# Kernel tuning notes

Hardware: AMD Instinct MI355X
Metric: run time of the kernel (lower is better)

Reference implementation:

```python
import jax, jax.numpy as jnp
import numpy as np

EPS = 1e-6
D_MODEL, D_HEAD, COND_F = 1024, 64, 768
N_HEADS = D_MODEL // D_HEAD
BATCH, SEQ = 2, 2048


def _rope_freqs(d_head, n_heads):
    # RoPE.__init__: dim = d_head // 2; count = n_heads * dim // 4 = n_heads * d_head // 8
    d8 = d_head // 8
    log_min, log_max = np.log(np.pi), np.log(10.0 * np.pi)
    f = np.exp(np.linspace(log_min, log_max, n_heads * d8 + 1, dtype=np.float64)[:-1])
    return jnp.asarray(f.reshape(d8, n_heads).T, dtype=jnp.float32)  # [nh, d8]


def _apply_rotary(x, theta):
    # x: [n, nh, l, e], theta: [n, nh, l, d8]; rotate first 2*d8 channels
    d = theta.shape[-1]
    x1, x2, rest = x[..., :d], x[..., d:2 * d], x[..., 2 * d:]
    cos, sin = jnp.cos(theta), jnp.sin(theta)
    y1 = x1 * cos - x2 * sin
    y2 = x2 * cos + x1 * sin
    return jnp.concatenate([y1, y2, rest], axis=-1)


def setup_inputs() -> dict:
    key = jax.random.key(0)
    ks = jax.random.split(key, 6)
    x = jax.random.normal(ks[0], (BATCH, SEQ, D_MODEL), dtype=jnp.float32)
    pos = jnp.broadcast_to(jnp.arange(SEQ, dtype=jnp.float32), (BATCH, SEQ))[..., None]
    cond = jax.random.normal(ks[1], (BATCH, COND_F), dtype=jnp.float32)
    w_norm = jax.random.normal(ks[2], (D_MODEL, COND_F), dtype=jnp.float32) * 0.02
    w_qkv = jax.random.normal(ks[3], (3 * D_MODEL, D_MODEL), dtype=jnp.float32) * 0.02
    scale = jnp.full((N_HEADS,), 10.0, dtype=jnp.float32)
    w_out = jax.random.normal(ks[4], (D_MODEL, D_MODEL), dtype=jnp.float32) * 0.02
    return {"x": x, "pos": pos, "cond": cond, "w_norm": w_norm,
            "w_qkv": w_qkv, "scale": scale, "w_out": w_out}


def reference(x, pos, cond, w_norm, w_qkv, scale, w_out):
    n, l, d = x.shape
    nh, e = N_HEADS, D_HEAD
    skip = x
    # AdaRMSNorm: scale = (linear(cond) + 1) * rsqrt(mean(x^2))
    cond_scale = cond @ w_norm.T + 1.0                      # [n, d]
    mean_sq = jnp.mean(x * x, axis=-1, keepdims=True)       # [n, l, 1]
    xn = x * (cond_scale[:, None, :] * jax.lax.rsqrt(mean_sq + EPS))
    # QKV projection
    qkv = (xn @ w_qkv.T).reshape(n, l, 3, nh, e)
    q = jnp.transpose(qkv[:, :, 0], (0, 2, 1, 3))           # [n, nh, l, e]
    k = jnp.transpose(qkv[:, :, 1], (0, 2, 1, 3))
    v = jnp.transpose(qkv[:, :, 2], (0, 2, 1, 3))
    # cosine-sim scaling
    sqrt_scale = jnp.sqrt(scale)[None, :, None, None]       # [1, nh, 1, 1]
    q = q * (sqrt_scale * jax.lax.rsqrt(jnp.sum(q * q, axis=-1, keepdims=True) + EPS))
    k = k * (sqrt_scale * jax.lax.rsqrt(jnp.sum(k * k, axis=-1, keepdims=True) + EPS))
    # RoPE: theta = pos[..., None] * freqs -> [n, l, nh, d8] -> [n, nh, l, d8]
    freqs = _rope_freqs(e, nh)
    theta = jnp.transpose(pos[..., None] * freqs, (0, 2, 1, 3))
    q = _apply_rotary(q, theta)
    k = _apply_rotary(k, theta)
    # attention with softmax scale = 1.0
    scores = jnp.einsum('nhle,nhme->nhlm', q, k)
    attn = jax.nn.softmax(scores, axis=-1)
    out = jnp.einsum('nhlm,nhme->nhle', attn, v)
    out = jnp.transpose(out, (0, 2, 1, 3)).reshape(n, l, d)
    return out @ w_out.T + skip
```

## Files before the change

kernel.cpp:

```cpp
#include <hip/hip_runtime.h>
#include <math.h>

#define D_MODEL 1024
#define D_HEAD  64
#define N_HEADS 16
#define COND_F  768
#define BATCH   2
#define SEQ     2048
#define NTOK    (BATCH*SEQ)
#define QKV_N   (3*D_MODEL)

typedef unsigned short u16;
typedef __attribute__((ext_vector_type(4))) float  f32x4;
typedef __attribute__((ext_vector_type(8))) __bf16 bfrag;
typedef __attribute__((ext_vector_type(4))) unsigned short u16x4;
typedef __attribute__((ext_vector_type(8))) unsigned short u16x8;

__device__ __forceinline__ u16 f2bf(float f) {
    unsigned u = __builtin_bit_cast(unsigned, f);
    return (u16)((u + 0x7fffu + ((u >> 16) & 1u)) >> 16);
}
__device__ __forceinline__ float bf2f(u16 h) {
    unsigned u = ((unsigned)h) << 16;
    return __builtin_bit_cast(float, u);
}

__device__ __forceinline__ float fexp2(float x) {
    float y;
    asm("v_exp_f32 %0, %1" : "=v"(y) : "v"(x));
    return y;
}

__device__ __forceinline__ void async16(const void* g, void* l) {
    __builtin_amdgcn_global_load_lds(
        (const __attribute__((address_space(1))) unsigned int*)g,
        (__attribute__((address_space(3))) unsigned int*)l, 16, 0, 0);
}

#define SBAR do { __builtin_amdgcn_sched_barrier(0); \
                  __builtin_amdgcn_s_barrier(); \
                  __builtin_amdgcn_sched_barrier(0); } while (0)
#define WAITV4 do { asm volatile("s_waitcnt vmcnt(4)" ::: "memory"); } while (0)
#define WAITV2 do { asm volatile("s_waitcnt vmcnt(2)" ::: "memory"); } while (0)
#define WAITV0 do { asm volatile("s_waitcnt vmcnt(0)" ::: "memory"); } while (0)

__global__ __launch_bounds__(256) void prep_kernel(const float* __restrict__ wqkv,
                                                   const float* __restrict__ wout,
                                                   u16* __restrict__ wqkv_b,
                                                   u16* __restrict__ wout_b,
                                                   const float* __restrict__ cond,
                                                   const float* __restrict__ w_norm,
                                                   float* __restrict__ cs,
                                                   const float* __restrict__ pos,
                                                   float2* __restrict__ tab) {
    if (blockIdx.x < 2048) {
        int i = blockIdx.x * 256 + threadIdx.x;
        const int n1 = QKV_N * D_MODEL / 8;
        const float* src; u16* dst; int off;
        if (i < n1) { src = wqkv; dst = wqkv_b; off = i * 8; }
        else        { src = wout; dst = wout_b; off = (i - n1) * 8; }
        float4 a = *(const float4*)(src + off);
        float4 b = *(const float4*)(src + off + 4);
        *(u16x4*)(dst + off)     = (u16x4){f2bf(a.x), f2bf(a.y), f2bf(a.z), f2bf(a.w)};
        *(u16x4*)(dst + off + 4) = (u16x4){f2bf(b.x), f2bf(b.y), f2bf(b.z), f2bf(b.w)};
    } else if (blockIdx.x < 2560) {
        int lane = threadIdx.x & 63, w = threadIdx.x >> 6;
        int wid = (blockIdx.x - 2048) * 4 + w;
        int b = wid >> 10, d = wid & 1023;
        const float* c = cond + b * COND_F;
        const float* wn = w_norm + (size_t)d * COND_F;
        float acc = 0.f;
        #pragma unroll
        for (int kk = 0; kk < 3; ++kk) {
            int j = kk * 256 + lane * 4;
            float4 cv = *(const float4*)(c + j);
            float4 wv = *(const float4*)(wn + j);
            acc += cv.x * wv.x + cv.y * wv.y + cv.z * wv.z + cv.w * wv.w;
        }
        for (int m = 1; m < 64; m <<= 1) acc += __shfl_xor(acc, m);
        if (lane == 0) cs[wid] = acc + 1.0f;
    } else {
        int i = (blockIdx.x - 2560) * 256 + threadIdx.x;
        int j = i & 7, h = (i >> 3) & 15;
        int s = (i >> 7) & 2047, b = i >> 18;
        double lf = 1.1447298858494001741 + (double)(j * 16 + h) * (2.302585092994045684 / 128.0);
        float fr = (float)exp(lf);
        float th = pos[b * SEQ + s] * fr;
        tab[i] = make_float2(cosf(th), sinf(th));
    }
}

__global__ __launch_bounds__(256) void rmsnorm_kernel(const float* __restrict__ x,
                                                      const float* __restrict__ cs,
                                                      u16* __restrict__ xn) {
    int tok = blockIdx.x, t = threadIdx.x;
    int b = tok >> 11;
    const float* xr = x + (size_t)tok * D_MODEL;
    float4 v = *(const float4*)(xr + t * 4);
    float ss = v.x * v.x + v.y * v.y + v.z * v.z + v.w * v.w;
    for (int m = 1; m < 64; m <<= 1) ss += __shfl_xor(ss, m);
    __shared__ float red[4];
    int w = t >> 6;
    if ((t & 63) == 0) red[w] = ss;
    __syncthreads();
    float tot = red[0] + red[1] + red[2] + red[3];
    float r = rsqrtf(tot * (1.0f / D_MODEL) + 1e-6f);
    float4 cv = *(const float4*)(cs + b * D_MODEL + t * 4);
    *(u16x4*)(xn + (size_t)tok * D_MODEL + t * 4) =
        (u16x4){f2bf(v.x * cv.x * r), f2bf(v.y * cv.y * r),
                f2bf(v.z * cv.z * r), f2bf(v.w * cv.w * r)};
}

__global__ __launch_bounds__(256) void gemm_qkv(const u16* __restrict__ A, const u16* __restrict__ B,
                                                u16* __restrict__ Cq, u16* __restrict__ Ck,
                                                u16* __restrict__ Cv,
                                                const float* __restrict__ scale,
                                                const float2* __restrict__ tab,
                                                int M, int N, int K) {
    __shared__ u16 As0[128 * 32];
    __shared__ u16 As1[128 * 32];
    __shared__ u16 Bs0[128 * 32];
    __shared__ u16 Bs1[128 * 32];
    int tid = threadIdx.x;
    int lane = tid & 63, w = tid >> 6;
    int wr = w >> 1, wc = w & 1;
    int m0 = blockIdx.x * 128, n0 = blockIdx.y * 128;
    f32x4 acc[4][4] = {};
    const u16* Ag = A + (size_t)m0 * K;
    const u16* Bg = B + (size_t)n0 * K;
    int lr = lane & 15, lq = lane >> 4;

    #define GSTAGE(kt, Ad, Bd) do { \
        _Pragma("unroll") \
        for (int i = 0; i < 2; ++i) { \
            int c = i * 256 + tid; int row = c >> 2, col = (c & 3) * 8; \
            async16(Ag + (size_t)row * K + (kt) + col, Ad + c * 8); \
            async16(Bg + (size_t)row * K + (kt) + col, Bd + c * 8); \
        } } while (0)

    auto compute = [&](const u16* Asb, const u16* Bsb) {
        bfrag af[4], bfv[4];
        #pragma unroll
        for (int fm = 0; fm < 4; ++fm)
            af[fm] = *(const bfrag*)&Asb[(wr * 64 + fm * 16 + lr) * 32 + lq * 8];
        #pragma unroll
        for (int fn = 0; fn < 4; ++fn)
            bfv[fn] = *(const bfrag*)&Bsb[(wc * 64 + fn * 16 + lr) * 32 + lq * 8];
        #pragma unroll
        for (int fm = 0; fm < 4; ++fm)
            #pragma unroll
            for (int fn = 0; fn < 4; ++fn)
                acc[fm][fn] = __builtin_amdgcn_mfma_f32_16x16x32_bf16(af[fm], bfv[fn], acc[fm][fn], 0, 0, 0);
    };

    const int NK = K / 32;
    GSTAGE(0, As0, Bs0);
    GSTAGE(32, As1, Bs1);

    for (int t = 0; t < NK; t += 2) {
        if (t + 1 < NK) WAITV4; else WAITV0;
        SBAR;
        compute(As0, Bs0);
        SBAR;
        if (t + 2 < NK) GSTAGE((size_t)(t + 2) * 32, As0, Bs0);
        if (t + 1 < NK) {
            if (t + 2 < NK) WAITV4; else WAITV0;
            SBAR;
            compute(As1, Bs1);
            SBAR;
            if (t + 3 < NK) GSTAGE((size_t)(t + 3) * 32, As1, Bs1);
        }
    }
    #undef GSTAGE

    #pragma unroll
    for (int fn_dummy = 0; fn_dummy < 1; ++fn_dummy) {
        int colbase0 = n0 + wc * 64;
        int sel = colbase0 >> 10;
        int h = (colbase0 >> 6) & 15;
        int bb = m0 >> 11;
        if (sel == 2) {
            #pragma unroll
            for (int fm = 0; fm < 4; ++fm) {
                int sP = (m0 & 2047) + wr * 64 + (fm >> 1) * 32 + 8 * lq + 4 * (fm & 1);
                #pragma unroll
                for (int fn = 0; fn < 4; ++fn) {
                    int e = fn * 16 + lr;
                    u16x4 pk = {f2bf(acc[fm][fn][0]), f2bf(acc[fm][fn][1]),
                                f2bf(acc[fm][fn][2]), f2bf(acc[fm][fn][3])};
                    *(u16x4*)&Cv[((size_t)(bb * N_HEADS + h) * D_HEAD + e) * SEQ + sP] = pk;
                }
            }
        } else {
            u16* p = sel ? Ck : Cq;
            float sq = sqrtf(scale[h]);
            float mult = (sel == 0) ? sq * 1.4426950408889634f : sq;
            #pragma unroll
            for (int fm = 0; fm < 4; ++fm) {
                int s0 = (m0 & 2047) + wr * 64 + fm * 16 + lq * 4;
                #pragma unroll
                for (int r = 0; r < 4; ++r) {
                    float v0 = acc[fm][0][r], v1 = acc[fm][1][r],
                          v2 = acc[fm][2][r], v3 = acc[fm][3][r];
                    float ss = v0 * v0 + v1 * v1 + v2 * v2 + v3 * v3;
                    ss += __shfl_xor(ss, 1); ss += __shfl_xor(ss, 2);
                    ss += __shfl_xor(ss, 4); ss += __shfl_xor(ss, 8);
                    float rs = mult * rsqrtf(ss + 1e-6f);
                    v0 *= rs; v1 *= rs; v2 *= rs; v3 *= rs;
                    float part = __shfl_xor(v0, 8);
                    float2 cs2 = tab[(((size_t)bb * SEQ + (s0 + r)) * 16 + h) * 8 + (lr & 7)];
                    v0 = (lr < 8) ? v0 * cs2.x - part * cs2.y
                                  : v0 * cs2.x + part * cs2.y;
                    size_t rp = ((size_t)(bb * N_HEADS + h) * SEQ + (s0 + r)) * D_HEAD;
                    p[rp + lr]      = f2bf(v0);
                    p[rp + 16 + lr] = f2bf(v1);
                    p[rp + 32 + lr] = f2bf(v2);
                    p[rp + 48 + lr] = f2bf(v3);
                }
            }
        }
    }
}

__global__ __launch_bounds__(512) void gemm_out(const u16* __restrict__ A, const u16* __restrict__ B,
                                                float* __restrict__ Cf,
                                                const float* __restrict__ skip,
                                                int M, int N, int K) {
    __shared__ u16 As0[128 * 32];
    __shared__ u16 As1[128 * 32];
    __shared__ u16 Bs0[128 * 32];
    __shared__ u16 Bs1[128 * 32];
    int tid = threadIdx.x;
    int lane = tid & 63, w = tid >> 6;
    int wr = w >> 1, wc = w & 1;
    int m0 = blockIdx.x * 128, n0 = blockIdx.y * 128;
    f32x4 acc[2][4] = {};
    const u16* Ag = A + (size_t)m0 * K;
    const u16* Bg = B + (size_t)n0 * K;
    int lr = lane & 15, lq = lane >> 4;

    int srow = tid >> 2, scol = (tid & 3) * 8;

    #define GSTAGE(kt, Ad, Bd) do { \
        async16(Ag + (size_t)srow * K + (kt) + scol, Ad + tid * 8); \
        async16(Bg + (size_t)srow * K + (kt) + scol, Bd + tid * 8); } while (0)

    auto compute = [&](const u16* Asb, const u16* Bsb) {
        bfrag af[2], bfv[4];
        #pragma unroll
        for (int fm = 0; fm < 2; ++fm)
            af[fm] = *(const bfrag*)&Asb[(wr * 32 + fm * 16 + lr) * 32 + lq * 8];
        #pragma unroll
        for (int fn = 0; fn < 4; ++fn)
            bfv[fn] = *(const bfrag*)&Bsb[(wc * 64 + fn * 16 + lr) * 32 + lq * 8];
        #pragma unroll
        for (int fm = 0; fm < 2; ++fm)
            #pragma unroll
            for (int fn = 0; fn < 4; ++fn)
                acc[fm][fn] = __builtin_amdgcn_mfma_f32_16x16x32_bf16(af[fm], bfv[fn], acc[fm][fn], 0, 0, 0);
    };

    const int NK = K / 32;
    GSTAGE(0, As0, Bs0);
    GSTAGE(32, As1, Bs1);

    for (int t = 0; t < NK; t += 2) {
        if (t + 1 < NK) WAITV2; else WAITV0;
        SBAR;
        compute(As0, Bs0);
        SBAR;
        if (t + 2 < NK) GSTAGE((size_t)(t + 2) * 32, As0, Bs0);
        if (t + 1 < NK) {
            if (t + 2 < NK) WAITV2; else WAITV0;
            SBAR;
            compute(As1, Bs1);
            SBAR;
            if (t + 3 < NK) GSTAGE((size_t)(t + 3) * 32, As1, Bs1);
        }
    }
    #undef GSTAGE

    #pragma unroll
    for (int fm = 0; fm < 2; ++fm) {
        int rowbase = m0 + wr * 32 + fm * 16 + lq * 4;
        #pragma unroll
        for (int fn = 0; fn < 4; ++fn) {
            int col = n0 + wc * 64 + fn * 16 + lr;
            #pragma unroll
            for (int r = 0; r < 4; ++r) {
                int row = rowbase + r;
                Cf[(size_t)row * N + col] = acc[fm][fn][r] + skip[(size_t)row * N + col];
            }
        }
    }
}

__global__ __launch_bounds__(512) void attn_kernel(const u16* __restrict__ q,
                                                   const u16* __restrict__ k,
                                                   const u16* __restrict__ vt,
                                                   u16* __restrict__ o_part,
                                                   float* __restrict__ lsum_part) {
    __shared__ u16 Ks0[64 * 64];
    __shared__ u16 Ks1[64 * 64];
    __shared__ u16 Vs0[64 * 64];
    __shared__ u16 Vs1[64 * 64];
    int tid = threadIdx.x, lane = tid & 63, w = tid >> 6;

    int rid = blockIdx.x;
    int nwg = gridDim.x, cpx = nwg >> 3;
    int wid = (rid & 7) * cpx + (rid >> 3);
    int xq = wid & 7;
    int rest = wid >> 3;
    int bh = rest & 31;
    int z = rest >> 5;
    int nz = nwg >> 8;
    int qs = xq * 256;
    int chunk = SEQ / nz;
    int kv0 = z * chunk;
    int lr = lane & 15, lq = lane >> 4;

    bfrag qf[2][2];
    #pragma unroll
    for (int mf = 0; mf < 2; ++mf) {
        const u16* qb = q + ((size_t)bh * SEQ + qs + w * 32 + mf * 16 + lr) * D_HEAD + lq * 8;
        qf[mf][0] = *(const bfrag*)qb;
        qf[mf][1] = *(const bfrag*)(qb + 32);
    }
    bfrag ones;
    #pragma unroll
    for (int j = 0; j < 8; ++j) ones[j] = (__bf16)1.0f;

    f32x4 oacc[2][4] = {};
    f32x4 oacc5[2] = {};
    const u16* kbase = k + (size_t)bh * SEQ * D_HEAD;
    const u16* vbase = vt + (size_t)bh * D_HEAD * SEQ;

    int srow = tid >> 3, scol = (tid & 7) ^ ((tid >> 3) & 7);
    const u16* kg = kbase + (size_t)srow * 64 + scol * 8;
    const u16* vg = vbase + (size_t)srow * SEQ + scol * 8;

    #define STAGE(kt, Kd, Vd) do { \
        async16(kg + (size_t)(kt) * 64, Kd + tid * 8); \
        async16(vg + (kt),              Vd + tid * 8); } while (0)

    auto tile_compute = [&](const u16* Kb, const u16* Vb) {
        f32x4 sacc[2][4] = {};
        __builtin_amdgcn_s_setprio(1);
        #pragma unroll
        for (int nb = 0; nb < 4; ++nb) {
            int row = nb * 16 + lr;
            #pragma unroll
            for (int kb = 0; kb < 2; ++kb) {
                bfrag kf = *(const bfrag*)&Kb[row * 64 + (((kb * 4 + lq) ^ (row & 7)) * 8)];
                sacc[0][nb] = __builtin_amdgcn_mfma_f32_16x16x32_bf16(kf, qf[0][kb], sacc[0][nb], 0, 0, 0);
                sacc[1][nb] = __builtin_amdgcn_mfma_f32_16x16x32_bf16(kf, qf[1][kb], sacc[1][nb], 0, 0, 0);
            }
        }
        __builtin_amdgcn_s_setprio(0);

        #pragma unroll
        for (int kb = 0; kb < 2; ++kb) {
            bfrag pf[2];
            #pragma unroll
            for (int mf = 0; mf < 2; ++mf)
                #pragma unroll
                for (int half = 0; half < 2; ++half) {
                    int nb = kb * 2 + half;
                    #pragma unroll
                    for (int r = 0; r < 4; ++r)
                        pf[mf][half * 4 + r] = (__bf16)fexp2(sacc[mf][nb][r]);
                }
            __builtin_amdgcn_s_setprio(1);
            oacc5[0] = __builtin_amdgcn_mfma_f32_16x16x32_bf16(pf[0], ones, oacc5[0], 0, 0, 0);
            oacc5[1] = __builtin_amdgcn_mfma_f32_16x16x32_bf16(pf[1], ones, oacc5[1], 0, 0, 0);
            #pragma unroll
            for (int eb = 0; eb < 4; ++eb) {
                int row = eb * 16 + lr;
                bfrag vf = *(const bfrag*)&Vb[row * 64 + (((kb * 4 + lq) ^ (row & 7)) * 8)];
                oacc[0][eb] = __builtin_amdgcn_mfma_f32_16x16x32_bf16(pf[0], vf, oacc[0][eb], 0, 0, 0);
                oacc[1][eb] = __builtin_amdgcn_mfma_f32_16x16x32_bf16(pf[1], vf, oacc[1][eb], 0, 0, 0);
            }
            __builtin_amdgcn_s_setprio(0);
        }
    };

    STAGE(kv0, Ks0, Vs0);
    asm volatile("s_waitcnt vmcnt(0)" ::: "memory");
    __syncthreads();

    const int NTILE = chunk / 64;
    for (int t = 0; t < NTILE; t += 2) {
        if (t + 1 < NTILE) STAGE(kv0 + (t + 1) * 64, Ks1, Vs1);
        tile_compute(Ks0, Vs0);
        __syncthreads();
        if (t + 2 < NTILE) STAGE(kv0 + (t + 2) * 64, Ks0, Vs0);
        if (t + 1 < NTILE) {
            tile_compute(Ks1, Vs1);
            __syncthreads();
        }
    }
    #undef STAGE

    int b = bh >> 4, h = bh & 15;
    u16* op = o_part + (size_t)z * NTOK * D_MODEL;
    #pragma unroll
    for (int mf = 0; mf < 2; ++mf) {
        #pragma unroll
        for (int r = 0; r < 4; ++r) {
            int qrow = qs + w * 32 + mf * 16 + lq * 4 + r;
            if (lr == 0)
                lsum_part[((size_t)z * BATCH * N_HEADS + bh) * SEQ + qrow] = oacc5[mf][r];
            #pragma unroll
            for (int eb = 0; eb < 4; ++eb) {
                int e = eb * 16 + lr;
                op[((size_t)b * SEQ + qrow) * D_MODEL + h * D_HEAD + e] = f2bf(oacc[mf][eb][r]);
            }
        }
    }
}

__global__ __launch_bounds__(256) void combine_kernel(const u16* __restrict__ o_part,
                                                      const float* __restrict__ lsum_part,
                                                      u16* __restrict__ out, int Z) {
    int i = blockIdx.x * 256 + threadIdx.x;
    int base = i * 8;
    int t = base >> 10, col = base & 1023;
    int b = t >> 11, s = t & 2047, h = col >> 6;
    size_t li = (size_t)(b * N_HEADS + h) * SEQ + s;
    float lsum = 0.f;
    for (int z = 0; z < Z; ++z) lsum += lsum_part[(size_t)z * BATCH * N_HEADS * SEQ + li];
    float inv = 1.0f / lsum;
    float acc[8] = {};
    for (int z = 0; z < Z; ++z) {
        u16x8 a = *(const u16x8*)(o_part + (size_t)z * NTOK * D_MODEL + base);
        #pragma unroll
        for (int j = 0; j < 8; ++j) acc[j] += bf2f(a[j]);
    }
    u16x8 r;
    #pragma unroll
    for (int j = 0; j < 8; ++j) r[j] = f2bf(acc[j] * inv);
    *(u16x8*)(out + base) = r;
}

extern "C" void kernel_launch(void* const* d_in, const int* in_sizes, int n_in,
                              void* d_out, int out_size, void* d_ws, size_t ws_size,
                              hipStream_t stream) {
    const float* x      = (const float*)d_in[0];
    const float* pos    = (const float*)d_in[1];
    const float* cond   = (const float*)d_in[2];
    const float* w_norm = (const float*)d_in[3];
    const float* w_qkv  = (const float*)d_in[4];
    const float* scale  = (const float*)d_in[5];
    const float* w_out  = (const float*)d_in[6];
    float* out = (float*)d_out;

    char* ws = (char*)d_ws;
    u16* xn     = (u16*)ws;
    u16* wqkv_b = (u16*)(ws + (8u  << 20));
    u16* wout_b = (u16*)(ws + (14u << 20));
    float* cs   = (float*)(ws + (16u << 20));
    u16* qb     = (u16*)(ws + (16u << 20) + (1u << 16));
    const size_t HSZ = (size_t)BATCH * N_HEADS * SEQ * D_HEAD;
    u16* kb = qb + HSZ;
    u16* vt = kb + HSZ;
    u16* o_part   = (u16*)(ws + (41u << 20));
    float2* tab   = (float2*)(ws + (41u << 20));
    u16* attn_o = xn;

    size_t need4 = (41ull << 20) + 4 * ((size_t)NTOK * D_MODEL * 2) + 4 * ((size_t)BATCH * N_HEADS * SEQ * 4);
    int Z = (ws_size >= need4) ? 4 : 2;
    float* lsum_p = (float*)(ws + (41u << 20) + (size_t)Z * NTOK * D_MODEL * 2);

    prep_kernel<<<dim3(4608), dim3(256), 0, stream>>>(w_qkv, w_out, wqkv_b, wout_b,
                                                      cond, w_norm, cs, pos, (float2*)tab);
    rmsnorm_kernel<<<dim3(NTOK), dim3(256), 0, stream>>>(x, cs, xn);
    gemm_qkv<<<dim3(NTOK / 128, QKV_N / 128), dim3(256), 0, stream>>>(
        xn, wqkv_b, qb, kb, vt, scale, (const float2*)tab, NTOK, QKV_N, D_MODEL);
    attn_kernel<<<dim3(256 * Z), dim3(512), 0, stream>>>(
        qb, kb, vt, o_part, lsum_p);
    combine_kernel<<<dim3(NTOK * D_MODEL / 8 / 256), dim3(256), 0, stream>>>(o_part, lsum_p, attn_o, Z);
    gemm_out<<<dim3(NTOK / 128, D_MODEL / 128), dim3(512), 0, stream>>>(
        attn_o, wout_b, out, x, NTOK, D_MODEL, D_MODEL);
}
```

Before: 127.0 us.

## Widen QKV GEMM tile to 128x256 and triple-buffer output GEMM

```diff
diff --git a/kernel.cpp b/kernel.cpp
--- a/kernel.cpp
+++ b/kernel.cpp
@@ -41,6 +41,7 @@
                   __builtin_amdgcn_s_barrier(); \
                   __builtin_amdgcn_sched_barrier(0); } while (0)
 #define WAITV4 do { asm volatile("s_waitcnt vmcnt(4)" ::: "memory"); } while (0)
+#define WAITV3 do { asm volatile("s_waitcnt vmcnt(3)" ::: "memory"); } while (0)
 #define WAITV2 do { asm volatile("s_waitcnt vmcnt(2)" ::: "memory"); } while (0)
 #define WAITV0 do { asm volatile("s_waitcnt vmcnt(0)" ::: "memory"); } while (0)
 
@@ -111,7 +112,7 @@
                 f2bf(v.z * cv.z * r), f2bf(v.w * cv.w * r)};
 }
 
-__global__ __launch_bounds__(256) void gemm_qkv(const u16* __restrict__ A, const u16* __restrict__ B,
+__global__ __launch_bounds__(512) void gemm_qkv(const u16* __restrict__ A, const u16* __restrict__ B,
                                                 u16* __restrict__ Cq, u16* __restrict__ Ck,
                                                 u16* __restrict__ Cv,
                                                 const float* __restrict__ scale,
@@ -119,24 +120,23 @@
                                                 int M, int N, int K) {
     __shared__ u16 As0[128 * 32];
     __shared__ u16 As1[128 * 32];
-    __shared__ u16 Bs0[128 * 32];
-    __shared__ u16 Bs1[128 * 32];
+    __shared__ u16 Bs0[256 * 32];
+    __shared__ u16 Bs1[256 * 32];
     int tid = threadIdx.x;
     int lane = tid & 63, w = tid >> 6;
-    int wr = w >> 1, wc = w & 1;
-    int m0 = blockIdx.x * 128, n0 = blockIdx.y * 128;
+    int wr = w >> 2, wc = w & 3;
+    int m0 = blockIdx.x * 128, n0 = blockIdx.y * 256;
     f32x4 acc[4][4] = {};
     const u16* Ag = A + (size_t)m0 * K;
     const u16* Bg = B + (size_t)n0 * K;
     int lr = lane & 15, lq = lane >> 4;
 
+    int srow = tid >> 2, scol = (tid & 3) * 8;
+
     #define GSTAGE(kt, Ad, Bd) do { \
-        _Pragma("unroll") \
-        for (int i = 0; i < 2; ++i) { \
-            int c = i * 256 + tid; int row = c >> 2, col = (c & 3) * 8; \
-            async16(Ag + (size_t)row * K + (kt) + col, Ad + c * 8); \
-            async16(Bg + (size_t)row * K + (kt) + col, Bd + c * 8); \
-        } } while (0)
+        async16(Ag + (size_t)srow * K + (kt) + scol, Ad + tid * 8); \
+        async16(Bg + (size_t)srow * K + (kt) + scol, Bd + tid * 8); \
+        async16(Bg + (size_t)(srow + 128) * K + (kt) + scol, Bd + (512 + tid) * 8); } while (0)
 
     auto compute = [&](const u16* Asb, const u16* Bsb) {
         bfrag af[4], bfv[4];
@@ -158,13 +158,13 @@
     GSTAGE(32, As1, Bs1);
 
     for (int t = 0; t < NK; t += 2) {
-        if (t + 1 < NK) WAITV4; else WAITV0;
+        if (t + 1 < NK) WAITV3; else WAITV0;
         SBAR;
         compute(As0, Bs0);
         SBAR;
         if (t + 2 < NK) GSTAGE((size_t)(t + 2) * 32, As0, Bs0);
         if (t + 1 < NK) {
-            if (t + 2 < NK) WAITV4; else WAITV0;
+            if (t + 2 < NK) WAITV3; else WAITV0;
             SBAR;
             compute(As1, Bs1);
             SBAR;
@@ -173,50 +173,47 @@
     }
     #undef GSTAGE
 
-    #pragma unroll
-    for (int fn_dummy = 0; fn_dummy < 1; ++fn_dummy) {
-        int colbase0 = n0 + wc * 64;
-        int sel = colbase0 >> 10;
-        int h = (colbase0 >> 6) & 15;
-        int bb = m0 >> 11;
-        if (sel == 2) {
-            #pragma unroll
-            for (int fm = 0; fm < 4; ++fm) {
-                int sP = (m0 & 2047) + wr * 64 + (fm >> 1) * 32 + 8 * lq + 4 * (fm & 1);
-                #pragma unroll
-                for (int fn = 0; fn < 4; ++fn) {
-                    int e = fn * 16 + lr;
-                    u16x4 pk = {f2bf(acc[fm][fn][0]), f2bf(acc[fm][fn][1]),
-                                f2bf(acc[fm][fn][2]), f2bf(acc[fm][fn][3])};
-                    *(u16x4*)&Cv[((size_t)(bb * N_HEADS + h) * D_HEAD + e) * SEQ + sP] = pk;
-                }
-            }
-        } else {
-            u16* p = sel ? Ck : Cq;
-            float sq = sqrtf(scale[h]);
-            float mult = (sel == 0) ? sq * 1.4426950408889634f : sq;
-            #pragma unroll
-            for (int fm = 0; fm < 4; ++fm) {
-                int s0 = (m0 & 2047) + wr * 64 + fm * 16 + lq * 4;
-                #pragma unroll
-                for (int r = 0; r < 4; ++r) {
-                    float v0 = acc[fm][0][r], v1 = acc[fm][1][r],
-                          v2 = acc[fm][2][r], v3 = acc[fm][3][r];
-                    float ss = v0 * v0 + v1 * v1 + v2 * v2 + v3 * v3;
-                    ss += __shfl_xor(ss, 1); ss += __shfl_xor(ss, 2);
-                    ss += __shfl_xor(ss, 4); ss += __shfl_xor(ss, 8);
-                    float rs = mult * rsqrtf(ss + 1e-6f);
-                    v0 *= rs; v1 *= rs; v2 *= rs; v3 *= rs;
-                    float part = __shfl_xor(v0, 8);
-                    float2 cs2 = tab[(((size_t)bb * SEQ + (s0 + r)) * 16 + h) * 8 + (lr & 7)];
-                    v0 = (lr < 8) ? v0 * cs2.x - part * cs2.y
-                                  : v0 * cs2.x + part * cs2.y;
-                    size_t rp = ((size_t)(bb * N_HEADS + h) * SEQ + (s0 + r)) * D_HEAD;
-                    p[rp + lr]      = f2bf(v0);
-                    p[rp + 16 + lr] = f2bf(v1);
-                    p[rp + 32 + lr] = f2bf(v2);
-                    p[rp + 48 + lr] = f2bf(v3);
-                }
+    int colbase0 = n0 + wc * 64;
+    int sel = colbase0 >> 10;
+    int h = (colbase0 >> 6) & 15;
+    int bb = m0 >> 11;
+    if (sel == 2) {
+        #pragma unroll
+        for (int fm = 0; fm < 4; ++fm) {
+            int sP = (m0 & 2047) + wr * 64 + (fm >> 1) * 32 + 8 * lq + 4 * (fm & 1);
+            #pragma unroll
+            for (int fn = 0; fn < 4; ++fn) {
+                int e = fn * 16 + lr;
+                u16x4 pk = {f2bf(acc[fm][fn][0]), f2bf(acc[fm][fn][1]),
+                            f2bf(acc[fm][fn][2]), f2bf(acc[fm][fn][3])};
+                *(u16x4*)&Cv[((size_t)(bb * N_HEADS + h) * D_HEAD + e) * SEQ + sP] = pk;
+            }
+        }
+    } else {
+        u16* p = sel ? Ck : Cq;
+        float sq = sqrtf(scale[h]);
+        float mult = (sel == 0) ? sq * 1.4426950408889634f : sq;
+        #pragma unroll
+        for (int fm = 0; fm < 4; ++fm) {
+            int s0 = (m0 & 2047) + wr * 64 + fm * 16 + lq * 4;
+            #pragma unroll
+            for (int r = 0; r < 4; ++r) {
+                float v0 = acc[fm][0][r], v1 = acc[fm][1][r],
+                      v2 = acc[fm][2][r], v3 = acc[fm][3][r];
+                float ss = v0 * v0 + v1 * v1 + v2 * v2 + v3 * v3;
+                ss += __shfl_xor(ss, 1); ss += __shfl_xor(ss, 2);
+                ss += __shfl_xor(ss, 4); ss += __shfl_xor(ss, 8);
+                float rs = mult * rsqrtf(ss + 1e-6f);
+                v0 *= rs; v1 *= rs; v2 *= rs; v3 *= rs;
+                float part = __shfl_xor(v0, 8);
+                float2 cs2 = tab[(((size_t)bb * SEQ + (s0 + r)) * 16 + h) * 8 + (lr & 7)];
+                v0 = (lr < 8) ? v0 * cs2.x - part * cs2.y
+                              : v0 * cs2.x + part * cs2.y;
+                size_t rp = ((size_t)(bb * N_HEADS + h) * SEQ + (s0 + r)) * D_HEAD;
+                p[rp + lr]      = f2bf(v0);
+                p[rp + 16 + lr] = f2bf(v1);
+                p[rp + 32 + lr] = f2bf(v2);
+                p[rp + 48 + lr] = f2bf(v3);
             }
         }
     }
@@ -228,8 +225,10 @@
                                                 int M, int N, int K) {
     __shared__ u16 As0[128 * 32];
     __shared__ u16 As1[128 * 32];
+    __shared__ u16 As2[128 * 32];
     __shared__ u16 Bs0[128 * 32];
     __shared__ u16 Bs1[128 * 32];
+    __shared__ u16 Bs2[128 * 32];
     int tid = threadIdx.x;
     int lane = tid & 63, w = tid >> 6;
     int wr = w >> 1, wc = w & 1;
@@ -263,21 +262,16 @@
     const int NK = K / 32;
     GSTAGE(0, As0, Bs0);
     GSTAGE(32, As1, Bs1);
-
-    for (int t = 0; t < NK; t += 2) {
-        if (t + 1 < NK) WAITV2; else WAITV0;
-        SBAR;
-        compute(As0, Bs0);
-        SBAR;
-        if (t + 2 < NK) GSTAGE((size_t)(t + 2) * 32, As0, Bs0);
-        if (t + 1 < NK) {
-            if (t + 2 < NK) WAITV2; else WAITV0;
-            SBAR;
-            compute(As1, Bs1);
-            SBAR;
-            if (t + 3 < NK) GSTAGE((size_t)(t + 3) * 32, As1, Bs1);
-        }
-    }
+    GSTAGE(64, As2, Bs2);
+
+    for (int t = 0; t + 2 < NK - 2; t += 3) {
+        WAITV4; SBAR; compute(As0, Bs0); SBAR; GSTAGE((size_t)(t + 3) * 32, As0, Bs0);
+        WAITV4; SBAR; compute(As1, Bs1); SBAR; GSTAGE((size_t)(t + 4) * 32, As1, Bs1);
+        WAITV4; SBAR; compute(As2, Bs2); SBAR;
+        if (t + 5 < NK) GSTAGE((size_t)(t + 5) * 32, As2, Bs2);
+    }
+    WAITV2; SBAR; compute(As0, Bs0); SBAR;
+    WAITV0; SBAR; compute(As1, Bs1); SBAR;
     #undef GSTAGE
 
     #pragma unroll
@@ -474,7 +468,7 @@
     prep_kernel<<<dim3(4608), dim3(256), 0, stream>>>(w_qkv, w_out, wqkv_b, wout_b,
                                                       cond, w_norm, cs, pos, (float2*)tab);
     rmsnorm_kernel<<<dim3(NTOK), dim3(256), 0, stream>>>(x, cs, xn);
-    gemm_qkv<<<dim3(NTOK / 128, QKV_N / 128), dim3(256), 0, stream>>>(
+    gemm_qkv<<<dim3(NTOK / 128, QKV_N / 256), dim3(512), 0, stream>>>(
         xn, wqkv_b, qb, kb, vt, scale, (const float2*)tab, NTOK, QKV_N, D_MODEL);
     attn_kernel<<<dim3(256 * Z), dim3(512), 0, stream>>>(
         qb, kb, vt, o_part, lsum_p);
```

Result: faster. 114.8 us (-9.6%).
